# Performance work log

Measured on AMD Instinct MI355X. Metric: run time of the kernel, lower is better.

Reference implementation:

```python
import jax, jax.numpy as jnp
import numpy as np

HIDDEN = 1024
HEADS = 16
HEAD_DIM = 64
FFN = 4096
LAYERS = 8
QLEN = 9
PATCH = 4
PREFIX = PATCH + 1
LATENT = 64
NSTEPS = 4


def _rope_tables():
    # matches __init__: cos/sin for positions 0..QLEN-1, sin first half negated
    half = HEAD_DIM // 2
    inv = 1.0 / (10000.0 ** (np.arange(half, dtype=np.float64) / half))
    ang = np.arange(QLEN)[:, None] * inv[None, :]          # [QLEN, half]
    cos = np.concatenate([np.cos(ang), np.cos(ang)], -1)   # [QLEN, HEAD_DIM]
    sin = np.concatenate([-np.sin(ang), np.sin(ang)], -1)  # first half *= -1
    return jnp.asarray(cos, jnp.float32), jnp.asarray(sin, jnp.float32)

ROPE_COS, ROPE_SIN = _rope_tables()


def _rms(x):
    # norm weight * sqrt(hidden) is folded into the following projection
    return x * jax.lax.rsqrt(jnp.sum(x * x, -1, keepdims=True))


def setup_inputs() -> dict:
    key = jax.random.key(0)
    ks = jax.random.split(key, 16)
    s = 0.02
    return {
        "step": 2,
        "random": jax.random.normal(ks[0], (1, PATCH, LATENT), jnp.float32),
        "dit_hidden": jax.random.normal(ks[1], (1, 1, HIDDEN), jnp.float32),
        "feat_cond": jax.random.normal(ks[2], (2, PATCH, HIDDEN), jnp.float32),
        "cfg_value": jnp.array([2.5], jnp.float32),
        "cfg_value_minus": jnp.array([1.0 - 2.5], jnp.float32),
        "t_emb": jax.random.normal(ks[3], (NSTEPS, 1, 1, HIDDEN), jnp.float32) * s,
        "dt": jax.random.uniform(ks[4], (NSTEPS,), jnp.float32) * 0.3,
        "in_proj_w": jax.random.normal(ks[5], (HIDDEN, LATENT), jnp.float32) * s,
        "in_proj_b": jnp.zeros((HIDDEN,), jnp.float32),
        "qkv_w": jax.random.normal(ks[6], (LAYERS, 3 * HIDDEN, HIDDEN), jnp.float32) * s,
        "qkv_b": jnp.zeros((LAYERS, 3 * HIDDEN), jnp.float32),
        "o_w": jax.random.normal(ks[7], (LAYERS, HIDDEN, HIDDEN), jnp.float32) * s,
        "gate_up_w": jax.random.normal(ks[8], (LAYERS, 2 * FFN, HIDDEN), jnp.float32) * s,
        "down_w": jax.random.normal(ks[9], (LAYERS, HIDDEN, FFN), jnp.float32) * s,
        "out_proj_w": jax.random.normal(ks[10], (LATENT, HIDDEN), jnp.float32) * s,
        "out_proj_b": jnp.zeros((LATENT,), jnp.float32),
    }


def reference(step, random, dit_hidden, feat_cond, cfg_value, cfg_value_minus,
              t_emb, dt, in_proj_w, in_proj_b, qkv_w, qkv_b, o_w, gate_up_w,
              down_w, out_proj_w, out_proj_b):
    t = t_emb[step]                                     # [1,1,H]
    h = dit_hidden + t
    h = jnp.concatenate([h, t], 0)                      # [2,1,H]  (cond / uncond)
    x = random @ in_proj_w.T + in_proj_b                # [1,PATCH,H]
    x = jnp.concatenate([x, x], 0)                      # [2,PATCH,H]
    hs = jnp.concatenate([h, feat_cond, x], 1)          # [2,QLEN,H]

    for i in range(LAYERS):
        res = hs
        n = _rms(hs)
        qkv = (n @ qkv_w[i].T + qkv_b[i]).reshape(2, QLEN, 3 * HEADS, HEAD_DIM)
        qk, v = qkv[:, :, :2 * HEADS], qkv[:, :, 2 * HEADS:]
        # RoPE (rotate_half = swap halves; sign is in ROPE_SIN)
        x1, x2 = jnp.split(qk, 2, axis=-1)
        rot = jnp.concatenate([x2, x1], -1)
        qk = qk * ROPE_COS[None, :, None, :] + rot * ROPE_SIN[None, :, None, :]
        q, k = qk[:, :, :HEADS], qk[:, :, HEADS:]
        # head_dim**-0.25 scale already folded into q/k weights
        scores = jnp.einsum('bqhd,bkhd->bhqk', q, k)
        attn = jax.nn.softmax(scores, -1)
        o = jnp.einsum('bhqk,bkhd->bqhd', attn, v).reshape(2, QLEN, HIDDEN)
        hs = res + o @ o_w[i].T
        res = hs
        n = _rms(hs)
        gu = n @ gate_up_w[i].T
        g, u = jnp.split(gu, 2, -1)
        hs = res + (jax.nn.silu(g) * u) @ down_w[i].T

    out = _rms(hs[:, PREFIX:]) @ out_proj_w.T + out_proj_b   # [2,PATCH,LATENT]
    pos = out[:1].reshape(1, 1, -1)
    neg = out[1:].reshape(1, 1, -1)
    dot = jnp.sum(pos * neg, -1, keepdims=True)
    sq = jnp.sum(neg * neg, -1, keepdims=True)
    guided = cfg_value * pos + cfg_value_minus * (dot / sq) * neg
    return random + guided.reshape(1, PATCH, LATENT) * dt[step]
```

## Files before the change

### kernel.cpp

```cpp
#include <hip/hip_runtime.h>
#include <hip/hip_bf16.h>

#define ROWS 18
#define HID 1024

__device__ __forceinline__ float dot4(float4 a, float4 b){
  return fmaf(a.x,b.x, fmaf(a.y,b.y, fmaf(a.z,b.z, a.w*b.w)));
}

template<int K, int S, int G, int NC, int ACT, int CSTR, bool RMS, bool BIAS, bool ATOMIC>
__global__ __launch_bounds__(256)
void gemm18(const float* __restrict__ W, const float* __restrict__ act,
            const float* __restrict__ bias, float* __restrict__ out)
{
  constexpr int L   = 64 / G;
  constexpr int KB  = K / S;
  constexpr int PK  = (KB <= 512) ? KB : 512;
  constexpr int NP  = KB / PK;
  constexpr int CHUNK = 4 * L;
  constexpr int NCH = PK / CHUNK;
  constexpr int CPB = 4 * G * NC;

  __shared__ float s_act[ROWS][PK];
  __shared__ float s_red[4 * G * NC * ROWS];
  __shared__ float s_scale[ROWS];

  const int tid  = threadIdx.x;
  const int w    = tid >> 6;
  const int lane = tid & 63;
  const int g    = (G == 1) ? 0 : (lane / L);
  const int l    = (G == 1) ? lane : (lane % L);
  const int cb   = blockIdx.x * CPB + (w * G + g) * NC;
  const int k0   = blockIdx.y * KB;

  float acc[NC][ROWS];
  #pragma unroll
  for (int i = 0; i < NC; i++)
    #pragma unroll
    for (int r = 0; r < ROWS; r++) acc[i][r] = 0.f;

  float rs[5];
  #pragma unroll
  for (int t = 0; t < 5; t++) rs[t] = 0.f;

  for (int p = 0; p < NP; p++) {
    __syncthreads();
    constexpr int N4 = ROWS * PK / 4;
    for (int t4 = tid; t4 < N4; t4 += 256) {
      const int r  = t4 / (PK / 4);
      const int k4 = (t4 % (PK / 4)) * 4;
      const int kg = k0 + p * PK + k4;
      float4 v;
      if (ACT == 0) {
        v = *(const float4*)&act[(size_t)r * K + kg];
      } else {
        float4 gv = *(const float4*)&act[(size_t)r * 8192 + kg];
        float4 uv = *(const float4*)&act[(size_t)r * 8192 + 4096 + kg];
        v.x = gv.x / (1.f + __expf(-gv.x)) * uv.x;
        v.y = gv.y / (1.f + __expf(-gv.y)) * uv.y;
        v.z = gv.z / (1.f + __expf(-gv.z)) * uv.z;
        v.w = gv.w / (1.f + __expf(-gv.w)) * uv.w;
      }
      *(float4*)&s_act[r][k4] = v;
    }
    __syncthreads();

    if (RMS) {
      #pragma unroll
      for (int t = 0; t < 5; t++) {
        const int r = w + 4 * t;
        if (r < ROWS) {
          float ss = 0.f;
          for (int kk = 4 * lane; kk < PK; kk += 256) {
            float4 a = *(const float4*)&s_act[r][kk];
            ss += dot4(a, a);
          }
          rs[t] += ss;
        }
      }
    }

    #pragma unroll
    for (int ch = 0; ch < NCH; ch++) {
      const int kk = ch * CHUNK + 4 * l;
      float4 wv[NC];
      #pragma unroll
      for (int i = 0; i < NC; i++)
        wv[i] = *(const float4*)&W[(size_t)(cb + i) * K + k0 + p * PK + kk];
      #pragma unroll
      for (int r = 0; r < ROWS; r++) {
        float4 a = *(const float4*)&s_act[r][kk];
        #pragma unroll
        for (int i = 0; i < NC; i++)
          acc[i][r] = fmaf(wv[i].x, a.x, fmaf(wv[i].y, a.y,
                      fmaf(wv[i].z, a.z, fmaf(wv[i].w, a.w, acc[i][r]))));
      }
    }
  }

  if (RMS) {
    #pragma unroll
    for (int t = 0; t < 5; t++) {
      const int r = w + 4 * t;
      if (r < ROWS) {
        float ss = rs[t];
        #pragma unroll
        for (int m = 32; m >= 1; m >>= 1) ss += __shfl_xor(ss, m);
        if (lane == 0) s_scale[r] = rsqrtf(ss);
      }
    }
  }

  #pragma unroll
  for (int i = 0; i < NC; i++)
    #pragma unroll
    for (int r = 0; r < ROWS; r++) {
      float v = acc[i][r];
      #pragma unroll
      for (int m = L / 2; m >= 1; m >>= 1) v += __shfl_xor(v, m);
      if (l == 0) s_red[((w * G + g) * NC + i) * ROWS + r] = v;
    }
  __syncthreads();

  constexpr int TOT = 4 * G * NC * ROWS;
  for (int t = tid; t < TOT; t += 256) {
    const int r    = t % ROWS;
    const int rest = t / ROWS;
    const int c    = blockIdx.x * CPB + rest;
    float v = s_red[rest * ROWS + r];
    if (RMS)  v *= s_scale[r];
    if (BIAS) v += bias[c];
    if (ATOMIC) atomicAdd(&out[(size_t)r * CSTR + c], v);
    else        out[(size_t)r * CSTR + c] = v;
  }
}

__global__ __launch_bounds__(256)
void prep_kernel(const int* __restrict__ step, const float* __restrict__ random_,
                 const float* __restrict__ dit_hidden, const float* __restrict__ feat_cond,
                 const float* __restrict__ t_emb, const float* __restrict__ in_w,
                 const float* __restrict__ in_b, float* __restrict__ hs)
{
  const int c = blockIdx.x * 256 + threadIdx.x;
  const int st = step[0];
  const float tv = t_emb[(size_t)st * HID + c];
  hs[0 * HID + c] = dit_hidden[c] + tv;
  hs[9 * HID + c] = tv;
  #pragma unroll
  for (int p = 0; p < 4; p++) {
    hs[(1 + p) * HID + c]     = feat_cond[(0 * 4 + p) * HID + c];
    hs[(9 + 1 + p) * HID + c] = feat_cond[(1 * 4 + p) * HID + c];
  }
  #pragma unroll
  for (int p = 0; p < 4; p++) {
    float a = in_b[c];
    #pragma unroll
    for (int q4 = 0; q4 < 16; q4++) {
      float4 wv = *(const float4*)&in_w[c * 64 + q4 * 4];
      float4 rv = *(const float4*)&random_[p * 64 + q4 * 4];
      a += dot4(wv, rv);
    }
    hs[(5 + p) * HID + c]     = a;
    hs[(9 + 5 + p) * HID + c] = a;
  }
}

__global__ __launch_bounds__(64)
void attn_kernel(const float* __restrict__ qkv, float* __restrict__ attn_out)
{
  const int bh = blockIdx.x;
  const int b = bh >> 4, h = bh & 15;
  const int d = threadIdx.x;
  const float* base = qkv + (size_t)b * 9 * 3072;
  float q[9], k[9], v[9];
  #pragma unroll
  for (int i = 0; i < 9; i++) {
    q[i] = base[i * 3072 + h * 64 + d];
    k[i] = base[i * 3072 + (16 + h) * 64 + d];
    v[i] = base[i * 3072 + (32 + h) * 64 + d];
  }
  const int j = d & 31;
  const float inv = powf(10000.f, -(float)j * (1.f / 32.f));
  #pragma unroll
  for (int i = 0; i < 9; i++) {
    const float ang = (float)i * inv;
    float sn, cs;
    sincosf(ang, &sn, &cs);
    const float sgn = (d < 32) ? -sn : sn;
    const float rq = __shfl_xor(q[i], 32);
    const float rk = __shfl_xor(k[i], 32);
    q[i] = q[i] * cs + rq * sgn;
    k[i] = k[i] * cs + rk * sgn;
  }
  float* obase = attn_out + (size_t)b * 9 * HID + h * 64 + d;
  for (int i = 0; i < 9; i++) {
    float sc[9];
    #pragma unroll
    for (int jj = 0; jj < 9; jj++) {
      float p = q[i] * k[jj];
      #pragma unroll
      for (int m = 32; m >= 1; m >>= 1) p += __shfl_xor(p, m);
      sc[jj] = p;
    }
    float mx = sc[0];
    #pragma unroll
    for (int jj = 1; jj < 9; jj++) mx = fmaxf(mx, sc[jj]);
    float den = 0.f;
    #pragma unroll
    for (int jj = 0; jj < 9; jj++) { sc[jj] = __expf(sc[jj] - mx); den += sc[jj]; }
    float o = 0.f;
    #pragma unroll
    for (int jj = 0; jj < 9; jj++) o += sc[jj] * v[jj];
    obase[i * HID] = o / den;
  }
}

__global__ __launch_bounds__(256)
void outproj_kernel(const float* __restrict__ hs, const float* __restrict__ W,
                    const float* __restrict__ bias, float* __restrict__ out_tmp)
{
  const int c = blockIdx.x, t = threadIdx.x;
  const int w = t >> 6, lane = t & 63;
  const float4 w4 = *(const float4*)&W[(size_t)c * HID + t * 4];
  __shared__ float la[8][4], ls[8][4];
  #pragma unroll
  for (int r8 = 0; r8 < 8; r8++) {
    const int row = (r8 >> 2) * 9 + 5 + (r8 & 3);
    const float4 h4 = *(const float4*)&hs[(size_t)row * HID + t * 4];
    float a = dot4(w4, h4), s = dot4(h4, h4);
    #pragma unroll
    for (int m = 32; m >= 1; m >>= 1) { a += __shfl_xor(a, m); s += __shfl_xor(s, m); }
    if (lane == 0) { la[r8][w] = a; ls[r8][w] = s; }
  }
  __syncthreads();
  if (t < 8) {
    const float a = la[t][0] + la[t][1] + la[t][2] + la[t][3];
    const float s = ls[t][0] + ls[t][1] + ls[t][2] + ls[t][3];
    out_tmp[t * 64 + c] = a * rsqrtf(s) + bias[c];
  }
}

__global__ __launch_bounds__(256)
void combine_kernel(const float* __restrict__ out_tmp, const float* __restrict__ random_,
                    const float* __restrict__ cfg, const float* __restrict__ cfgm,
                    const float* __restrict__ dt, const int* __restrict__ step,
                    float* __restrict__ dout)
{
  const int t = threadIdx.x;
  const int w = t >> 6, lane = t & 63;
  const float pos = out_tmp[t], neg = out_tmp[256 + t];
  float d = pos * neg, s = neg * neg;
  #pragma unroll
  for (int m = 32; m >= 1; m >>= 1) { d += __shfl_xor(d, m); s += __shfl_xor(s, m); }
  __shared__ float ld[4], lsq[4];
  if (lane == 0) { ld[w] = d; lsq[w] = s; }
  __syncthreads();
  const float dot = ld[0] + ld[1] + ld[2] + ld[3];
  const float sq  = lsq[0] + lsq[1] + lsq[2] + lsq[3];
  const float guided = cfg[0] * pos + cfgm[0] * (dot / sq) * neg;
  dout[t] = random_[t] + guided * dt[step[0]];
}

extern "C" void kernel_launch(void* const* d_in, const int* in_sizes, int n_in,
                              void* d_out, int out_size, void* d_ws, size_t ws_size,
                              hipStream_t stream)
{
  const int*   step   = (const int*)  d_in[0];
  const float* random_= (const float*)d_in[1];
  const float* dit_h  = (const float*)d_in[2];
  const float* feat   = (const float*)d_in[3];
  const float* cfg    = (const float*)d_in[4];
  const float* cfgm   = (const float*)d_in[5];
  const float* t_emb  = (const float*)d_in[6];
  const float* dt     = (const float*)d_in[7];
  const float* in_w   = (const float*)d_in[8];
  const float* in_b   = (const float*)d_in[9];
  const float* qkv_w  = (const float*)d_in[10];
  const float* qkv_b  = (const float*)d_in[11];
  const float* o_w    = (const float*)d_in[12];
  const float* gu_w   = (const float*)d_in[13];
  const float* dn_w   = (const float*)d_in[14];
  const float* op_w   = (const float*)d_in[15];
  const float* op_b   = (const float*)d_in[16];

  float* hs     = (float*)d_ws;
  float* qkvb   = hs    + ROWS * HID;
  float* attnb  = qkvb  + ROWS * 3072;
  float* gub    = attnb + ROWS * HID;
  float* outtmp = gub   + ROWS * 8192;

  prep_kernel<<<4, 256, 0, stream>>>(step, random_, dit_h, feat, t_emb, in_w, in_b, hs);

  for (int i = 0; i < 8; i++) {
    const float* qw = qkv_w + (size_t)i * 3072 * 1024;
    const float* qb = qkv_b + (size_t)i * 3072;
    const float* ow = o_w   + (size_t)i * 1024 * 1024;
    const float* gw = gu_w  + (size_t)i * 8192 * 1024;
    const float* dw = dn_w  + (size_t)i * 1024 * 4096;

    gemm18<1024, 1, 1, 4, 0, 3072, true,  true,  false>
        <<<dim3(192, 1), 256, 0, stream>>>(qw, hs, qb, qkvb);
    attn_kernel<<<32, 64, 0, stream>>>(qkvb, attnb);
    gemm18<1024, 4, 1, 4, 0, 1024, false, false, true>
        <<<dim3(64, 4), 256, 0, stream>>>(ow, attnb, nullptr, hs);
    gemm18<1024, 1, 2, 4, 0, 8192, true,  false, false>
        <<<dim3(256, 1), 256, 0, stream>>>(gw, hs, nullptr, gub);
    gemm18<4096, 4, 1, 4, 1, 1024, false, false, true>
        <<<dim3(64, 4), 256, 0, stream>>>(dw, gub, nullptr, hs);
  }

  outproj_kernel<<<64, 256, 0, stream>>>(hs, op_w, op_b, outtmp);
  combine_kernel<<<1, 256, 0, stream>>>(outtmp, random_, cfg, cfgm, dt, step, (float*)d_out);
}
```

Measured before the change: 952.5 us.

## Restructure GEMV kernels with register prefetch, split-K QKV, fused SiLU and output head

Rewrites the skinny GEMM kernel so each wave owns four weight rows, with weight loads for the next K chunk issued into registers before the FMAs on the current chunk. The QKV projection becomes split-K into two partial buffers that the attention kernel sums. The gate/up projection gets a dedicated 512-thread kernel that pairs gate and up rows in one block and applies SiLU*up in its epilogue, so the down projection reads a ready 4096-wide activation. The out-projection and CFG combine merge into a single one-block kernel, and RMS sums are computed directly from global memory. This trades more registers and a single-block tail kernel for better memory-latency hiding and fewer launches.

```diff
diff --git a/kernel.cpp b/kernel.cpp
--- a/kernel.cpp
+++ b/kernel.cpp
@@ -7,95 +7,90 @@
 __device__ __forceinline__ float dot4(float4 a, float4 b){
   return fmaf(a.x,b.x, fmaf(a.y,b.y, fmaf(a.z,b.z, a.w*b.w)));
 }
-
-template<int K, int S, int G, int NC, int ACT, int CSTR, bool RMS, bool BIAS, bool ATOMIC>
+__device__ __forceinline__ void fma4(float& acc, float4 w, float4 a){
+  acc = fmaf(w.x,a.x, fmaf(w.y,a.y, fmaf(w.z,a.z, fmaf(w.w,a.w, acc))));
+}
+
+template<int K, int ASTR, int KB, int PK, int CSTR, bool RMS, bool BIAS, bool ATOMIC, bool SPLITBUF>
 __global__ __launch_bounds__(256)
-void gemm18(const float* __restrict__ W, const float* __restrict__ act,
-            const float* __restrict__ bias, float* __restrict__ out)
-{
-  constexpr int L   = 64 / G;
-  constexpr int KB  = K / S;
-  constexpr int PK  = (KB <= 512) ? KB : 512;
+void gemm_k(const float* __restrict__ Wt, const float* __restrict__ act,
+            const float* __restrict__ bias, float* __restrict__ outp)
+{
   constexpr int NP  = KB / PK;
-  constexpr int CHUNK = 4 * L;
-  constexpr int NCH = PK / CHUNK;
-  constexpr int CPB = 4 * G * NC;
-
-  __shared__ float s_act[ROWS][PK];
-  __shared__ float s_red[4 * G * NC * ROWS];
-  __shared__ float s_scale[ROWS];
+  constexpr int NCH = PK / 256;
+  static_assert(NP <= 2, "");
+
+  __shared__ float sact[ROWS * PK];
+  __shared__ float sred[16 * ROWS];
+  __shared__ float sscale[ROWS];
 
   const int tid  = threadIdx.x;
   const int w    = tid >> 6;
   const int lane = tid & 63;
-  const int g    = (G == 1) ? 0 : (lane / L);
-  const int l    = (G == 1) ? lane : (lane % L);
-  const int cb   = blockIdx.x * CPB + (w * G + g) * NC;
+  const int cb   = blockIdx.x * 16;
   const int k0   = blockIdx.y * KB;
 
-  float acc[NC][ROWS];
-  #pragma unroll
-  for (int i = 0; i < NC; i++)
+  float4 wva[NCH * 4], wvb[NCH * 4];
+  float  acc[4][ROWS];
+  #pragma unroll
+  for (int i = 0; i < 4; i++)
     #pragma unroll
     for (int r = 0; r < ROWS; r++) acc[i][r] = 0.f;
 
-  float rs[5];
-  #pragma unroll
-  for (int t = 0; t < 5; t++) rs[t] = 0.f;
-
-  for (int p = 0; p < NP; p++) {
-    __syncthreads();
+  auto wissue = [&](float4* wv, int p) {
+    #pragma unroll
+    for (int ch = 0; ch < NCH; ch++)
+      #pragma unroll
+      for (int i = 0; i < 4; i++)
+        wv[ch * 4 + i] = *(const float4*)&Wt[(size_t)(cb + w * 4 + i) * K +
+                                             k0 + p * PK + ch * 256 + 4 * lane];
+  };
+  auto stage = [&](int p) {
     constexpr int N4 = ROWS * PK / 4;
     for (int t4 = tid; t4 < N4; t4 += 256) {
       const int r  = t4 / (PK / 4);
       const int k4 = (t4 % (PK / 4)) * 4;
-      const int kg = k0 + p * PK + k4;
-      float4 v;
-      if (ACT == 0) {
-        v = *(const float4*)&act[(size_t)r * K + kg];
-      } else {
-        float4 gv = *(const float4*)&act[(size_t)r * 8192 + kg];
-        float4 uv = *(const float4*)&act[(size_t)r * 8192 + 4096 + kg];
-        v.x = gv.x / (1.f + __expf(-gv.x)) * uv.x;
-        v.y = gv.y / (1.f + __expf(-gv.y)) * uv.y;
-        v.z = gv.z / (1.f + __expf(-gv.z)) * uv.z;
-        v.w = gv.w / (1.f + __expf(-gv.w)) * uv.w;
+      *(float4*)&sact[r * PK + k4] =
+          *(const float4*)&act[(size_t)r * ASTR + k0 + p * PK + k4];
+    }
+  };
+  auto dofma = [&](const float4* wv) {
+    #pragma unroll
+    for (int ch = 0; ch < NCH; ch++)
+      #pragma unroll
+      for (int r = 0; r < ROWS; r++) {
+        float4 a = *(const float4*)&sact[r * PK + ch * 256 + 4 * lane];
+        #pragma unroll
+        for (int i = 0; i < 4; i++) fma4(acc[i][r], wv[ch * 4 + i], a);
       }
-      *(float4*)&s_act[r][k4] = v;
-    }
-    __syncthreads();
-
-    if (RMS) {
-      #pragma unroll
-      for (int t = 0; t < 5; t++) {
-        const int r = w + 4 * t;
-        if (r < ROWS) {
-          float ss = 0.f;
-          for (int kk = 4 * lane; kk < PK; kk += 256) {
-            float4 a = *(const float4*)&s_act[r][kk];
-            ss += dot4(a, a);
-          }
-          rs[t] += ss;
+  };
+
+  wissue(wva, 0);
+
+  float rs[5] = {0.f,0.f,0.f,0.f,0.f};
+  if (RMS) {
+    #pragma unroll
+    for (int t = 0; t < 5; t++) {
+      const int r = w + 4 * t;
+      if (r < ROWS) {
+        #pragma unroll
+        for (int kk = 4 * lane; kk < K; kk += 256) {
+          float4 a = *(const float4*)&act[(size_t)r * ASTR + kk];
+          rs[t] += dot4(a, a);
         }
       }
     }
-
-    #pragma unroll
-    for (int ch = 0; ch < NCH; ch++) {
-      const int kk = ch * CHUNK + 4 * l;
-      float4 wv[NC];
-      #pragma unroll
-      for (int i = 0; i < NC; i++)
-        wv[i] = *(const float4*)&W[(size_t)(cb + i) * K + k0 + p * PK + kk];
-      #pragma unroll
-      for (int r = 0; r < ROWS; r++) {
-        float4 a = *(const float4*)&s_act[r][kk];
-        #pragma unroll
-        for (int i = 0; i < NC; i++)
-          acc[i][r] = fmaf(wv[i].x, a.x, fmaf(wv[i].y, a.y,
-                      fmaf(wv[i].z, a.z, fmaf(wv[i].w, a.w, acc[i][r]))));
-      }
-    }
+  }
+
+  stage(0);
+  __syncthreads();
+  if (NP > 1) wissue(wvb, 1);
+  dofma(wva);
+  if (NP > 1) {
+    __syncthreads();
+    stage(1);
+    __syncthreads();
+    dofma(wvb);
   }
 
   if (RMS) {
@@ -106,32 +101,136 @@
         float ss = rs[t];
         #pragma unroll
         for (int m = 32; m >= 1; m >>= 1) ss += __shfl_xor(ss, m);
-        if (lane == 0) s_scale[r] = rsqrtf(ss);
+        if (lane == 0) sscale[r] = rsqrtf(ss);
       }
     }
   }
 
   #pragma unroll
-  for (int i = 0; i < NC; i++)
+  for (int i = 0; i < 4; i++)
     #pragma unroll
     for (int r = 0; r < ROWS; r++) {
       float v = acc[i][r];
       #pragma unroll
-      for (int m = L / 2; m >= 1; m >>= 1) v += __shfl_xor(v, m);
-      if (l == 0) s_red[((w * G + g) * NC + i) * ROWS + r] = v;
-    }
-  __syncthreads();
-
-  constexpr int TOT = 4 * G * NC * ROWS;
-  for (int t = tid; t < TOT; t += 256) {
+      for (int m = 32; m >= 1; m >>= 1) v += __shfl_xor(v, m);
+      if (lane == 0) sred[(w * 4 + i) * ROWS + r] = v;
+    }
+  __syncthreads();
+
+  float* op = outp + (SPLITBUF ? (size_t)blockIdx.y * ROWS * CSTR : 0);
+  for (int t = tid; t < 16 * ROWS; t += 256) {
     const int r    = t % ROWS;
     const int rest = t / ROWS;
-    const int c    = blockIdx.x * CPB + rest;
-    float v = s_red[rest * ROWS + r];
-    if (RMS)  v *= s_scale[r];
-    if (BIAS) v += bias[c];
-    if (ATOMIC) atomicAdd(&out[(size_t)r * CSTR + c], v);
-    else        out[(size_t)r * CSTR + c] = v;
+    const int c    = cb + rest;
+    float v = sred[rest * ROWS + r];
+    if (RMS)  v *= sscale[r];
+    if (BIAS) { if (blockIdx.y == 0) v += bias[c]; }
+    if (ATOMIC) atomicAdd(&op[(size_t)r * CSTR + c], v);
+    else        op[(size_t)r * CSTR + c] = v;
+  }
+}
+
+__global__ __launch_bounds__(512)
+void gu_kernel(const float* __restrict__ Wt, const float* __restrict__ act,
+               float* __restrict__ gub)
+{
+  __shared__ float sact[ROWS * 512];
+  __shared__ float sred[32 * ROWS];
+  __shared__ float sscale[ROWS];
+
+  const int tid  = threadIdx.x;
+  const int w    = tid >> 6;
+  const int lane = tid & 63;
+  const int cb   = blockIdx.x * 16;
+  const int wrow0 = (w >= 4 ? 4096 : 0) + cb + (w & 3) * 4;
+
+  float4 wva[8], wvb[8];
+  float  acc[4][ROWS];
+  #pragma unroll
+  for (int i = 0; i < 4; i++)
+    #pragma unroll
+    for (int r = 0; r < ROWS; r++) acc[i][r] = 0.f;
+
+  auto wissue = [&](float4* wv, int p) {
+    #pragma unroll
+    for (int ch = 0; ch < 2; ch++)
+      #pragma unroll
+      for (int i = 0; i < 4; i++)
+        wv[ch * 4 + i] = *(const float4*)&Wt[(size_t)(wrow0 + i) * 1024 +
+                                             p * 512 + ch * 256 + 4 * lane];
+  };
+  auto stage = [&](int p) {
+    for (int t4 = tid; t4 < ROWS * 128; t4 += 512) {
+      const int r  = t4 / 128;
+      const int k4 = (t4 % 128) * 4;
+      *(float4*)&sact[r * 512 + k4] =
+          *(const float4*)&act[(size_t)r * 1024 + p * 512 + k4];
+    }
+  };
+  auto dofma = [&](const float4* wv) {
+    #pragma unroll
+    for (int ch = 0; ch < 2; ch++)
+      #pragma unroll
+      for (int r = 0; r < ROWS; r++) {
+        float4 a = *(const float4*)&sact[r * 512 + ch * 256 + 4 * lane];
+        #pragma unroll
+        for (int i = 0; i < 4; i++) fma4(acc[i][r], wv[ch * 4 + i], a);
+      }
+  };
+
+  wissue(wva, 0);
+
+  float rs[3] = {0.f, 0.f, 0.f};
+  #pragma unroll
+  for (int t = 0; t < 3; t++) {
+    const int r = w + 8 * t;
+    if (r < ROWS) {
+      #pragma unroll
+      for (int kk = 4 * lane; kk < 1024; kk += 256) {
+        float4 a = *(const float4*)&act[(size_t)r * 1024 + kk];
+        rs[t] += dot4(a, a);
+      }
+    }
+  }
+
+  stage(0);
+  __syncthreads();
+  wissue(wvb, 1);
+  dofma(wva);
+  __syncthreads();
+  stage(1);
+  __syncthreads();
+  dofma(wvb);
+
+  #pragma unroll
+  for (int t = 0; t < 3; t++) {
+    const int r = w + 8 * t;
+    if (r < ROWS) {
+      float ss = rs[t];
+      #pragma unroll
+      for (int m = 32; m >= 1; m >>= 1) ss += __shfl_xor(ss, m);
+      if (lane == 0) sscale[r] = rsqrtf(ss);
+    }
+  }
+
+  #pragma unroll
+  for (int i = 0; i < 4; i++)
+    #pragma unroll
+    for (int r = 0; r < ROWS; r++) {
+      float v = acc[i][r];
+      #pragma unroll
+      for (int m = 32; m >= 1; m >>= 1) v += __shfl_xor(v, m);
+      if (lane == 0) sred[(w * 4 + i) * ROWS + r] = v;
+    }
+  __syncthreads();
+
+  for (int t = tid; t < 16 * ROWS; t += 512) {
+    const int r = t >> 4;
+    const int j = t & 15;
+    const float s = sscale[r];
+    const float g = sred[j * ROWS + r] * s;
+    const float u = sred[(16 + j) * ROWS + r] * s;
+    gub[(size_t)r * 4096 + cb + j] = (g / (1.f + __expf(-g))) * u;
   }
 }
 
@@ -148,36 +247,37 @@
   hs[9 * HID + c] = tv;
   #pragma unroll
   for (int p = 0; p < 4; p++) {
-    hs[(1 + p) * HID + c]     = feat_cond[(0 * 4 + p) * HID + c];
-    hs[(9 + 1 + p) * HID + c] = feat_cond[(1 * 4 + p) * HID + c];
+    hs[(1 + p) * HID + c]  = feat_cond[(size_t)(0 * 4 + p) * HID + c];
+    hs[(10 + p) * HID + c] = feat_cond[(size_t)(1 * 4 + p) * HID + c];
   }
   #pragma unroll
   for (int p = 0; p < 4; p++) {
     float a = in_b[c];
     #pragma unroll
     for (int q4 = 0; q4 < 16; q4++) {
-      float4 wv = *(const float4*)&in_w[c * 64 + q4 * 4];
+      float4 wv = *(const float4*)&in_w[(size_t)c * 64 + q4 * 4];
       float4 rv = *(const float4*)&random_[p * 64 + q4 * 4];
       a += dot4(wv, rv);
     }
-    hs[(5 + p) * HID + c]     = a;
-    hs[(9 + 5 + p) * HID + c] = a;
+    hs[(5 + p) * HID + c]  = a;
+    hs[(14 + p) * HID + c] = a;
   }
 }
 
 __global__ __launch_bounds__(64)
-void attn_kernel(const float* __restrict__ qkv, float* __restrict__ attn_out)
+void attn_kernel(const float* __restrict__ qkvp, float* __restrict__ attn_out)
 {
   const int bh = blockIdx.x;
   const int b = bh >> 4, h = bh & 15;
   const int d = threadIdx.x;
-  const float* base = qkv + (size_t)b * 9 * 3072;
+  const float* p0 = qkvp + (size_t)b * 9 * 3072;
+  const float* p1 = p0 + (size_t)ROWS * 3072;
   float q[9], k[9], v[9];
   #pragma unroll
   for (int i = 0; i < 9; i++) {
-    q[i] = base[i * 3072 + h * 64 + d];
-    k[i] = base[i * 3072 + (16 + h) * 64 + d];
-    v[i] = base[i * 3072 + (32 + h) * 64 + d];
+    q[i] = p0[i * 3072 + h * 64 + d]        + p1[i * 3072 + h * 64 + d];
+    k[i] = p0[i * 3072 + (16 + h) * 64 + d] + p1[i * 3072 + (16 + h) * 64 + d];
+    v[i] = p0[i * 3072 + (32 + h) * 64 + d] + p1[i * 3072 + (32 + h) * 64 + d];
   }
   const int j = d & 31;
   const float inv = powf(10000.f, -(float)j * (1.f / 32.f));
@@ -185,7 +285,7 @@
   for (int i = 0; i < 9; i++) {
     const float ang = (float)i * inv;
     float sn, cs;
-    sincosf(ang, &sn, &cs);
+    __sincosf(ang, &sn, &cs);
     const float sgn = (d < 32) ? -sn : sn;
     const float rq = __shfl_xor(q[i], 32);
     const float rk = __shfl_xor(k[i], 32);
@@ -215,79 +315,101 @@
   }
 }
 
-__global__ __launch_bounds__(256)
-void outproj_kernel(const float* __restrict__ hs, const float* __restrict__ W,
-                    const float* __restrict__ bias, float* __restrict__ out_tmp)
-{
-  const int c = blockIdx.x, t = threadIdx.x;
-  const int w = t >> 6, lane = t & 63;
-  const float4 w4 = *(const float4*)&W[(size_t)c * HID + t * 4];
-  __shared__ float la[8][4], ls[8][4];
-  #pragma unroll
-  for (int r8 = 0; r8 < 8; r8++) {
-    const int row = (r8 >> 2) * 9 + 5 + (r8 & 3);
-    const float4 h4 = *(const float4*)&hs[(size_t)row * HID + t * 4];
-    float a = dot4(w4, h4), s = dot4(h4, h4);
-    #pragma unroll
-    for (int m = 32; m >= 1; m >>= 1) { a += __shfl_xor(a, m); s += __shfl_xor(s, m); }
-    if (lane == 0) { la[r8][w] = a; ls[r8][w] = s; }
-  }
-  __syncthreads();
-  if (t < 8) {
-    const float a = la[t][0] + la[t][1] + la[t][2] + la[t][3];
-    const float s = ls[t][0] + ls[t][1] + ls[t][2] + ls[t][3];
-    out_tmp[t * 64 + c] = a * rsqrtf(s) + bias[c];
-  }
-}
-
-__global__ __launch_bounds__(256)
-void combine_kernel(const float* __restrict__ out_tmp, const float* __restrict__ random_,
+__global__ __launch_bounds__(512)
+void outcomb_kernel(const float* __restrict__ hs, const float* __restrict__ opw,
+                    const float* __restrict__ opb, const float* __restrict__ random_,
                     const float* __restrict__ cfg, const float* __restrict__ cfgm,
                     const float* __restrict__ dt, const int* __restrict__ step,
                     float* __restrict__ dout)
 {
-  const int t = threadIdx.x;
-  const int w = t >> 6, lane = t & 63;
-  const float pos = out_tmp[t], neg = out_tmp[256 + t];
-  float d = pos * neg, s = neg * neg;
-  #pragma unroll
-  for (int m = 32; m >= 1; m >>= 1) { d += __shfl_xor(d, m); s += __shfl_xor(s, m); }
-  __shared__ float ld[4], lsq[4];
-  if (lane == 0) { ld[w] = d; lsq[w] = s; }
-  __syncthreads();
-  const float dot = ld[0] + ld[1] + ld[2] + ld[3];
-  const float sq  = lsq[0] + lsq[1] + lsq[2] + lsq[3];
-  const float guided = cfg[0] * pos + cfgm[0] * (dot / sq) * neg;
-  dout[t] = random_[t] + guided * dt[step[0]];
+  __shared__ float sh[8 * 1024];
+  __shared__ float sscale[8];
+  __shared__ float sout[512];
+  __shared__ float sdot[4], ssq[4];
+
+  const int tid = threadIdx.x;
+  const int w = tid >> 6, lane = tid & 63;
+
+  for (int t4 = tid; t4 < 2048; t4 += 512) {
+    const int r8 = t4 / 256;
+    const int k4 = (t4 % 256) * 4;
+    const int row = (r8 >> 2) * 9 + 5 + (r8 & 3);
+    *(float4*)&sh[r8 * 1024 + k4] = *(const float4*)&hs[(size_t)row * 1024 + k4];
+  }
+  __syncthreads();
+
+  {
+    float ss = 0.f;
+    #pragma unroll
+    for (int qq = 0; qq < 4; qq++) {
+      float4 a = *(const float4*)&sh[w * 1024 + 4 * lane + 256 * qq];
+      ss += dot4(a, a);
+    }
+    #pragma unroll
+    for (int m = 32; m >= 1; m >>= 1) ss += __shfl_xor(ss, m);
+    if (lane == 0) sscale[w] = rsqrtf(ss);
+  }
+  __syncthreads();
+
+  {
+    const int r8 = tid & 7;
+    const int c  = tid >> 3;
+    float a0 = 0.f, a1 = 0.f;
+    #pragma unroll 4
+    for (int k4 = 0; k4 < 128; k4++) {
+      a0 += dot4(*(const float4*)&sh[r8 * 1024 + 8 * k4],
+                 *(const float4*)&opw[(size_t)c * 1024 + 8 * k4]);
+      a1 += dot4(*(const float4*)&sh[r8 * 1024 + 8 * k4 + 4],
+                 *(const float4*)&opw[(size_t)c * 1024 + 8 * k4 + 4]);
+    }
+    sout[r8 * 64 + c] = (a0 + a1) * sscale[r8] + opb[c];
+  }
+  __syncthreads();
+
+  float pos = 0.f, neg = 0.f, dd = 0.f, sq = 0.f;
+  if (tid < 256) {
+    pos = sout[tid]; neg = sout[256 + tid];
+    dd = pos * neg; sq = neg * neg;
+  }
+  #pragma unroll
+  for (int m = 32; m >= 1; m >>= 1) { dd += __shfl_xor(dd, m); sq += __shfl_xor(sq, m); }
+  if (w < 4 && lane == 0) { sdot[w] = dd; ssq[w] = sq; }
+  __syncthreads();
+  if (tid < 256) {
+    const float dot = sdot[0] + sdot[1] + sdot[2] + sdot[3];
+    const float sqs = ssq[0] + ssq[1] + ssq[2] + ssq[3];
+    const float guided = cfg[0] * pos + cfgm[0] * (dot / sqs) * neg;
+    dout[tid] = random_[tid] + guided * dt[step[0]];
+  }
 }
 
 extern "C" void kernel_launch(void* const* d_in, const int* in_sizes, int n_in,
                               void* d_out, int out_size, void* d_ws, size_t ws_size,
                               hipStream_t stream)
 {
-  const int*   step   = (const int*)  d_in[0];
-  const float* random_= (const float*)d_in[1];
-  const float* dit_h  = (const float*)d_in[2];
-  const float* feat   = (const float*)d_in[3];
-  const float* cfg    = (const float*)d_in[4];
-  const float* cfgm   = (const float*)d_in[5];
-  const float* t_emb  = (const float*)d_in[6];
-  const float* dt     = (const float*)d_in[7];
-  const float* in_w   = (const float*)d_in[8];
-  const float* in_b   = (const float*)d_in[9];
-  const float* qkv_w  = (const float*)d_in[10];
-  const float* qkv_b  = (const float*)d_in[11];
-  const float* o_w    = (const float*)d_in[12];
-  const float* gu_w   = (const float*)d_in[13];
-  const float* dn_w   = (const float*)d_in[14];
-  const float* op_w   = (const float*)d_in[15];
-  const float* op_b   = (const float*)d_in[16];
-
-  float* hs     = (float*)d_ws;
-  float* qkvb   = hs    + ROWS * HID;
-  float* attnb  = qkvb  + ROWS * 3072;
-  float* gub    = attnb + ROWS * HID;
-  float* outtmp = gub   + ROWS * 8192;
+  const int*   step    = (const int*)  d_in[0];
+  const float* random_ = (const float*)d_in[1];
+  const float* dit_h   = (const float*)d_in[2];
+  const float* feat    = (const float*)d_in[3];
+  const float* cfg     = (const float*)d_in[4];
+  const float* cfgm    = (const float*)d_in[5];
+  const float* t_emb   = (const float*)d_in[6];
+  const float* dt      = (const float*)d_in[7];
+  const float* in_w    = (const float*)d_in[8];
+  const float* in_b    = (const float*)d_in[9];
+  const float* qkv_w   = (const float*)d_in[10];
+  const float* qkv_b   = (const float*)d_in[11];
+  const float* o_w     = (const float*)d_in[12];
+  const float* gu_w    = (const float*)d_in[13];
+  const float* dn_w    = (const float*)d_in[14];
+  const float* op_w    = (const float*)d_in[15];
+  const float* op_b    = (const float*)d_in[16];
+
+  float* hs    = (float*)d_ws;
+  float* qkvp  = hs   + ROWS * HID;
+  float* attnb = qkvp + 2 * ROWS * 3072;
+  float* gub   = attnb + ROWS * HID;
+  float* dout  = (float*)d_out;
 
   prep_kernel<<<4, 256, 0, stream>>>(step, random_, dit_h, feat, t_emb, in_w, in_b, hs);
 
@@ -298,17 +420,16 @@
     const float* gw = gu_w  + (size_t)i * 8192 * 1024;
     const float* dw = dn_w  + (size_t)i * 1024 * 4096;
 
-    gemm18<1024, 1, 1, 4, 0, 3072, true,  true,  false>
-        <<<dim3(192, 1), 256, 0, stream>>>(qw, hs, qb, qkvb);
-    attn_kernel<<<32, 64, 0, stream>>>(qkvb, attnb);
-    gemm18<1024, 4, 1, 4, 0, 1024, false, false, true>
+    gemm_k<1024, 1024, 512, 512, 3072, true, true, false, true>
+        <<<dim3(192, 2), 256, 0, stream>>>(qw, hs, qb, qkvp);
+    attn_kernel<<<32, 64, 0, stream>>>(qkvp, attnb);
+    gemm_k<1024, 1024, 256, 256, 1024, false, false, true, false>
         <<<dim3(64, 4), 256, 0, stream>>>(ow, attnb, nullptr, hs);
-    gemm18<1024, 1, 2, 4, 0, 8192, true,  false, false>
-        <<<dim3(256, 1), 256, 0, stream>>>(gw, hs, nullptr, gub);
-    gemm18<4096, 4, 1, 4, 1, 1024, false, false, true>
+    gu_kernel<<<256, 512, 0, stream>>>(gw, hs, gub);
+    gemm_k<4096, 4096, 1024, 512, 1024, false, false, true, false>
         <<<dim3(64, 4), 256, 0, stream>>>(dw, gub, nullptr, hs);
   }
 
-  outproj_kernel<<<64, 256, 0, stream>>>(hs, op_w, op_b, outtmp);
-  combine_kernel<<<1, 256, 0, stream>>>(outtmp, random_, cfg, cfgm, dt, step, (float*)d_out);
-}
+  outcomb_kernel<<<1, 512, 0, stream>>>(hs, op_w, op_b, random_, cfg, cfgm, dt,
+                                        step, dout);
+}
```

Measured after the change: 948.2 us. About the same (-0.4%).
